# Kernel optimization log

Hardware: AMD Instinct MI355X
Metric: run time of the kernel (lower is better)

Reference implementation:

```python
import jax, jax.numpy as jnp
import numpy as np

D_K = 64

def setup_inputs() -> dict:
    key = jax.random.key(0)
    ks = jax.random.split(key, 8)
    B, C, H, W = 4, 256, 40, 40
    d_k, d_g, n_rel = 64, 64, 16
    s = lambda fan_in: 1.0 / np.sqrt(fan_in)
    return {
        "x":  jax.random.normal(ks[0], (B, C, H, W), jnp.float32),
        "Wq": jax.random.normal(ks[1], (C, d_k), jnp.float32) * s(C),
        "bq": jnp.zeros((d_k,), jnp.float32),
        "Wk": jax.random.normal(ks[2], (C, d_k), jnp.float32) * s(C),
        "bk": jnp.zeros((d_k,), jnp.float32),
        "Wv": jax.random.normal(ks[3], (C, C), jnp.float32) * s(C),
        "bv": jnp.zeros((C,), jnp.float32),
        "Wg1": jax.random.normal(ks[4], (4, d_g), jnp.float32) * s(4),
        "bg1": jnp.zeros((d_g,), jnp.float32),
        "Wg2": jax.random.normal(ks[5], (d_g, d_g), jnp.float32) * s(d_g),
        "bg2": jnp.zeros((d_g,), jnp.float32),
        "Wgr": jax.random.normal(ks[6], (d_g, n_rel), jnp.float32) * s(d_g),
        "bgr": jnp.zeros((n_rel,), jnp.float32),
    }

def reference(x, Wq, bq, Wk, bk, Wv, bv, Wg1, bg1, Wg2, bg2, Wgr, bgr):
    B, C, H, W = x.shape
    N = H * W
    # [B, N, C] feature tokens
    feats = jnp.transpose(x, (0, 2, 3, 1)).reshape(B, N, C)
    # pseudo-bboxes: (x, y, 1, 1) per pixel
    yy, xx = jnp.meshgrid(jnp.arange(H), jnp.arange(W), indexing="ij")
    bboxes = jnp.stack(
        [xx.astype(jnp.float32), yy.astype(jnp.float32),
         jnp.ones((H, W), jnp.float32), jnp.ones((H, W), jnp.float32)],
        axis=-1).reshape(N, 4)
    # pairwise geometric features [N, N, 4]: diff[m, n] = bboxes[n] - bboxes[m]
    diff = bboxes[None, :, :] - bboxes[:, None, :]
    geo = jnp.log(jnp.abs(diff) + 1e-8)
    # geo embedding MLP -> relation weights
    e = jax.nn.relu(geo @ Wg1 + bg1)            # [N, N, d_g]
    e = jax.nn.relu(e @ Wg2 + bg2)              # [N, N, d_g]
    w_g = jax.nn.relu(e @ Wgr + bgr)            # [N, N, n_rel]
    w_g_mean = w_g.mean(axis=2)                 # [N, N]
    # appearance attention
    q = feats @ Wq + bq                         # [B, N, d_k]
    k = feats @ Wk + bk                         # [B, N, d_k]
    w_a = jax.nn.softmax(jnp.einsum("bnd,bmd->bnm", q, k) / jnp.sqrt(jnp.float32(D_K)), axis=2)
    w_mn = w_a * w_g_mean[None]                 # [B, N, N]
    v = feats @ Wv + bv                         # [B, N, C]
    rel = jnp.einsum("bnm,bmc->bnc", w_mn, v)
    aug = feats + rel
    return jnp.transpose(aug.reshape(B, H, W, C), (0, 3, 1, 2))
```

## Files before the change

kernel.cpp:

```cpp
#include <hip/hip_runtime.h>
#include <hip/hip_bf16.h>
#include <math.h>

#define NTOK 1600
#define CDIM 256
#define DK   64

typedef __attribute__((ext_vector_type(8))) short bf16x8;
typedef __attribute__((ext_vector_type(4))) float f32x4;

__device__ inline unsigned short f2bf(float v) {
    unsigned int u = __float_as_uint(v);
    unsigned int r = (u + 0x7fffu + ((u >> 16) & 1u)) >> 16;
    return (unsigned short)r;
}

__global__ __launch_bounds__(256) void geo_table_kernel(
    const float* __restrict__ W1, const float* __restrict__ b1,
    const float* __restrict__ W2, const float* __restrict__ b2,
    const float* __restrict__ Wgr, const float* __restrict__ bgr,
    float* __restrict__ table)
{
    __shared__ float e1s[4][64];
    __shared__ float e2s[4][64];
    int t = threadIdx.x;
    int w = t >> 6, j = t & 63;
    int idx = blockIdx.x * 4 + w;
    int ady = idx / 40, adx = idx % 40;
    float g0 = logf((float)adx + 1e-8f);
    float g1 = logf((float)ady + 1e-8f);
    float gc = logf(1e-8f);

    float e1 = fmaxf(g0*W1[j] + g1*W1[64+j] + gc*(W1[128+j]+W1[192+j]) + b1[j], 0.f);
    e1s[w][j] = e1;
    __syncthreads();

    float e2 = b2[j];
    #pragma unroll 8
    for (int i = 0; i < 64; ++i) e2 += e1s[w][i] * W2[i*64 + j];
    e2 = fmaxf(e2, 0.f);
    e2s[w][j] = e2;
    __syncthreads();

    int r = j & 15, q = j >> 4;
    float v = (q == 0) ? bgr[r] : 0.f;
    #pragma unroll
    for (int i = 0; i < 16; ++i) v += e2s[w][q*16 + i] * Wgr[(q*16 + i)*16 + r];
    v += __shfl_xor(v, 16); v += __shfl_xor(v, 32);
    v = fmaxf(v, 0.f);
    v += __shfl_xor(v, 1); v += __shfl_xor(v, 2);
    v += __shfl_xor(v, 4); v += __shfl_xor(v, 8);
    if (j == 0) table[idx] = v * (1.f / 16.f);
}

__global__ __launch_bounds__(256) void qkv_kernel(
    const float* __restrict__ x,
    const float* __restrict__ Wq, const float* __restrict__ bq,
    const float* __restrict__ Wk, const float* __restrict__ bk,
    const float* __restrict__ Wv, const float* __restrict__ bv,
    unsigned short* __restrict__ Qb, unsigned short* __restrict__ Kb,
    unsigned short* __restrict__ Vt)
{
    const int N = NTOK;
    int bx = blockIdx.x, jt = blockIdx.y, b = blockIdx.z;
    const float* Wm; const float* bias; int jb, stride;
    if (jt == 0)      { Wm = Wq; bias = bq; jb = 0;         stride = 64;  }
    else if (jt == 1) { Wm = Wk; bias = bk; jb = 0;         stride = 64;  }
    else              { Wm = Wv; bias = bv; jb = (jt-2)*64; stride = 256; }

    __shared__ __align__(16) unsigned short As[64*72];
    __shared__ __align__(16) unsigned short Bs[64*72];

    int t = threadIdx.x;
    int w = t >> 6, l = t & 63;
    int l15 = l & 15, l4 = l >> 4;
    int n0 = bx * 64;

    f32x4 acc[4];
    #pragma unroll
    for (int i = 0; i < 4; ++i) acc[i] = (f32x4){0.f,0.f,0.f,0.f};

    for (int kc = 0; kc < 4; ++kc) {
        int k0 = kc * 64;
        __syncthreads();
        #pragma unroll
        for (int p = 0; p < 4; ++p) {
            int k = p*16 + (t >> 4);
            int n4 = (t & 15) * 4;
            float4 xv = *(const float4*)&x[((size_t)(b*CDIM) + k0 + k)*N + n0 + n4];
            As[(n4+0)*72 + k] = f2bf(xv.x); As[(n4+1)*72 + k] = f2bf(xv.y);
            As[(n4+2)*72 + k] = f2bf(xv.z); As[(n4+3)*72 + k] = f2bf(xv.w);
            float4 wv = *(const float4*)&Wm[(size_t)(k0 + k)*stride + jb + n4];
            Bs[(n4+0)*72 + k] = f2bf(wv.x); Bs[(n4+1)*72 + k] = f2bf(wv.y);
            Bs[(n4+2)*72 + k] = f2bf(wv.z); Bs[(n4+3)*72 + k] = f2bf(wv.w);
        }
        __syncthreads();
        #pragma unroll
        for (int ks = 0; ks < 2; ++ks) {
            bf16x8 a = *(const bf16x8*)&As[(w*16 + l15)*72 + ks*32 + l4*8];
            #pragma unroll
            for (int jt4 = 0; jt4 < 4; ++jt4) {
                bf16x8 bf = *(const bf16x8*)&Bs[(jt4*16 + l15)*72 + ks*32 + l4*8];
                acc[jt4] = __builtin_amdgcn_mfma_f32_16x16x32_bf16(a, bf, acc[jt4], 0, 0, 0);
            }
        }
    }

    if (jt <= 1) {
        unsigned short* outb = (jt == 0 ? Qb : Kb) + (size_t)b*N*DK;
        float scale = (jt == 0) ? 0.125f : 1.0f;
        #pragma unroll
        for (int jt4 = 0; jt4 < 4; ++jt4) {
            int j = jt4*16 + l15;
            float bb = bias[j];
            #pragma unroll
            for (int r = 0; r < 4; ++r) {
                int n = n0 + w*16 + l4*4 + r;
                outb[(size_t)n*DK + j] = f2bf((acc[jt4][r] + bb) * scale);
            }
        }
    } else {
        __syncthreads();
        unsigned short* sv = (w < 2 ? As : Bs) + (w & 1) * (64*20);
        #pragma unroll
        for (int jt4 = 0; jt4 < 4; ++jt4) {
            int j = jt4*16 + l15;
            float bb = bias[jb + j];
            #pragma unroll
            for (int r = 0; r < 4; ++r)
                sv[j*20 + l4*4 + r] = f2bf(acc[jt4][r] + bb);
        }
        __syncthreads();
        int c = l;
        uint2 lo0 = *(const uint2*)&sv[c*20 + 0];
        uint2 lo1 = *(const uint2*)&sv[c*20 + 4];
        uint2 hi0 = *(const uint2*)&sv[c*20 + 8];
        uint2 hi1 = *(const uint2*)&sv[c*20 + 12];
        unsigned short* vrow = Vt + ((size_t)b*CDIM + jb + c)*N + n0 + w*16;
        *(uint4*)(vrow)     = make_uint4(lo0.x, lo0.y, lo1.x, lo1.y);
        *(uint4*)(vrow + 8) = make_uint4(hi0.x, hi0.y, hi1.x, hi1.y);
    }
}

__global__ __launch_bounds__(256) void attn_kernel(
    const float* __restrict__ x, const float* __restrict__ gtab,
    const unsigned short* __restrict__ Qb, const unsigned short* __restrict__ Kb,
    const unsigned short* __restrict__ Vt, float* __restrict__ out)
{
    const int N = NTOK, C = CDIM;
    int b = blockIdx.y, n0 = blockIdx.x * 16;
    int t = threadIdx.x;
    int w = t >> 6, l = t & 63;
    int l15 = l & 15, l4 = l >> 4;

    __shared__ __align__(16) unsigned short Pl[4][16*72];
    __shared__ float sh_g[NTOK];
    __shared__ float outs[16][260];
    __shared__ float zs[16];

    for (int p = t; p < NTOK; p += 256) sh_g[p] = gtab[p];
    for (int p = t; p < 16*260; p += 256) ((float*)outs)[p] = 0.f;
    if (t < 16) zs[t] = 0.f;

    const unsigned short* qrow = &Qb[((size_t)b*N + n0 + l15)*DK + l4*8];
    bf16x8 qa0 = *(const bf16x8*)qrow;
    bf16x8 qa1 = *(const bf16x8*)(qrow + 32);

    f32x4 acc[16];
    #pragma unroll
    for (int i = 0; i < 16; ++i) acc[i] = (f32x4){0.f,0.f,0.f,0.f};
    float z[4] = {0.f, 0.f, 0.f, 0.f};

    int yn[4], xn[4];
    #pragma unroll
    for (int r = 0; r < 4; ++r) {
        int n = n0 + l4*4 + r;
        yn[r] = n / 40; xn[r] = n - 40*yn[r];
    }

    __syncthreads();

    unsigned short* Pw = &Pl[w][0];

    for (int cc = w; cc < 25; cc += 4) {
        int m0 = cc * 64;
        #pragma unroll
        for (int tt = 0; tt < 4; ++tt) {
            int mg = m0 + tt*16 + l15;
            const unsigned short* kbase = &Kb[((size_t)b*N + mg)*DK + l4*8];
            bf16x8 kb0 = *(const bf16x8*)kbase;
            bf16x8 kb1 = *(const bf16x8*)(kbase + 32);
            f32x4 s4 = (f32x4){0.f,0.f,0.f,0.f};
            s4 = __builtin_amdgcn_mfma_f32_16x16x32_bf16(qa0, kb0, s4, 0, 0, 0);
            s4 = __builtin_amdgcn_mfma_f32_16x16x32_bf16(qa1, kb1, s4, 0, 0, 0);
            int ym = mg / 40, xm = mg - 40*ym;
            #pragma unroll
            for (int r = 0; r < 4; ++r) {
                float e = __expf(s4[r]);
                z[r] += e;
                int ady = ym - yn[r]; ady = ady < 0 ? -ady : ady;
                int adx = xm - xn[r]; adx = adx < 0 ? -adx : adx;
                Pw[(l4*4 + r)*72 + tt*16 + l15] = f2bf(e * sh_g[ady*40 + adx]);
            }
        }
        bf16x8 pa0 = *(const bf16x8*)&Pw[l15*72 + l4*8];
        bf16x8 pa1 = *(const bf16x8*)&Pw[l15*72 + 32 + l4*8];
        #pragma unroll
        for (int ct = 0; ct < 16; ++ct) {
            const unsigned short* vb = &Vt[((size_t)b*C + ct*16 + l15)*N + m0 + l4*8];
            bf16x8 v0 = *(const bf16x8*)vb;
            bf16x8 v1 = *(const bf16x8*)(vb + 32);
            acc[ct] = __builtin_amdgcn_mfma_f32_16x16x32_bf16(pa0, v0, acc[ct], 0, 0, 0);
            acc[ct] = __builtin_amdgcn_mfma_f32_16x16x32_bf16(pa1, v1, acc[ct], 0, 0, 0);
        }
    }

    #pragma unroll
    for (int r = 0; r < 4; ++r) {
        float v = z[r];
        v += __shfl_xor(v, 1); v += __shfl_xor(v, 2);
        v += __shfl_xor(v, 4); v += __shfl_xor(v, 8);
        if (l15 == 0) atomicAdd(&zs[l4*4 + r], v);
    }
    #pragma unroll
    for (int ct = 0; ct < 16; ++ct)
        #pragma unroll
        for (int r = 0; r < 4; ++r)
            atomicAdd(&outs[l4*4 + r][ct*16 + l15], acc[ct][r]);
    __syncthreads();

    int r2 = t & 15;
    float invz = 1.f / zs[r2];
    #pragma unroll
    for (int p = 0; p < 16; ++p) {
        int c2 = p*16 + (t >> 4);
        size_t gi = ((size_t)b*C + c2)*N + n0 + r2;
        out[gi] = x[gi] + outs[r2][c2] * invz;
    }
}

extern "C" void kernel_launch(void* const* d_in, const int* in_sizes, int n_in,
                              void* d_out, int out_size, void* d_ws, size_t ws_size,
                              hipStream_t stream)
{
    const float* x   = (const float*)d_in[0];
    const float* Wq  = (const float*)d_in[1];
    const float* bq  = (const float*)d_in[2];
    const float* Wk  = (const float*)d_in[3];
    const float* bk  = (const float*)d_in[4];
    const float* Wv  = (const float*)d_in[5];
    const float* bv  = (const float*)d_in[6];
    const float* Wg1 = (const float*)d_in[7];
    const float* bg1 = (const float*)d_in[8];
    const float* Wg2 = (const float*)d_in[9];
    const float* bg2 = (const float*)d_in[10];
    const float* Wgr = (const float*)d_in[11];
    const float* bgr = (const float*)d_in[12];

    char* ws = (char*)d_ws;
    float* table       = (float*)ws;
    unsigned short* Qb = (unsigned short*)(ws + 8192);
    unsigned short* Kb = (unsigned short*)(ws + 8192 + 819200);
    unsigned short* Vt = (unsigned short*)(ws + 8192 + 2*819200);

    geo_table_kernel<<<dim3(400), dim3(256), 0, stream>>>(Wg1, bg1, Wg2, bg2, Wgr, bgr, table);
    qkv_kernel<<<dim3(25, 6, 4), dim3(256), 0, stream>>>(x, Wq, bq, Wk, bk, Wv, bv, Qb, Kb, Vt);
    attn_kernel<<<dim3(100, 4), dim3(256), 0, stream>>>(x, table, Qb, Kb, Vt, (float*)d_out);
}
```

Before: 204.5 us.

## Use 8 waves per attention block over 32-key chunks and coalesce Vt stores

The attention kernel goes from 4 to 8 wavefronts per block, with each wave handling 32-key chunks (one MFMA per channel tile) instead of 64-key chunks. This doubles the in-block parallelism over keys and trims the per-iteration P buffer. In the QKV kernel, the transposed V tile is staged through one shared buffer with stride 68 and written back as fully coalesced 16-byte rows. The cost is more LDS atomics when the 8 waves reduce their partial outputs and more register pressure under the 512-thread launch bound.

```diff
diff --git a/kernel.cpp b/kernel.cpp
--- a/kernel.cpp
+++ b/kernel.cpp
@@ -121,28 +121,27 @@
         }
     } else {
         __syncthreads();
-        unsigned short* sv = (w < 2 ? As : Bs) + (w & 1) * (64*20);
+        unsigned short* sv = As;
         #pragma unroll
         for (int jt4 = 0; jt4 < 4; ++jt4) {
             int j = jt4*16 + l15;
             float bb = bias[jb + j];
             #pragma unroll
             for (int r = 0; r < 4; ++r)
-                sv[j*20 + l4*4 + r] = f2bf(acc[jt4][r] + bb);
-        }
-        __syncthreads();
-        int c = l;
-        uint2 lo0 = *(const uint2*)&sv[c*20 + 0];
-        uint2 lo1 = *(const uint2*)&sv[c*20 + 4];
-        uint2 hi0 = *(const uint2*)&sv[c*20 + 8];
-        uint2 hi1 = *(const uint2*)&sv[c*20 + 12];
-        unsigned short* vrow = Vt + ((size_t)b*CDIM + jb + c)*N + n0 + w*16;
-        *(uint4*)(vrow)     = make_uint4(lo0.x, lo0.y, lo1.x, lo1.y);
-        *(uint4*)(vrow + 8) = make_uint4(hi0.x, hi0.y, hi1.x, hi1.y);
-    }
-}
-
-__global__ __launch_bounds__(256) void attn_kernel(
+                sv[j*68 + w*16 + l4*4 + r] = f2bf(acc[jt4][r] + bb);
+        }
+        __syncthreads();
+        #pragma unroll
+        for (int p = 0; p < 2; ++p) {
+            int c   = p*32 + (t >> 3);
+            int off = (t & 7) * 8;
+            uint4 v = *(const uint4*)&sv[c*68 + off];
+            *(uint4*)&Vt[((size_t)b*CDIM + jb + c)*N + n0 + off] = v;
+        }
+    }
+}
+
+__global__ __launch_bounds__(512) void attn_kernel(
     const float* __restrict__ x, const float* __restrict__ gtab,
     const unsigned short* __restrict__ Qb, const unsigned short* __restrict__ Kb,
     const unsigned short* __restrict__ Vt, float* __restrict__ out)
@@ -153,13 +152,13 @@
     int w = t >> 6, l = t & 63;
     int l15 = l & 15, l4 = l >> 4;
 
-    __shared__ __align__(16) unsigned short Pl[4][16*72];
+    __shared__ __align__(16) unsigned short Pl[8][16*40];
     __shared__ float sh_g[NTOK];
     __shared__ float outs[16][260];
     __shared__ float zs[16];
 
-    for (int p = t; p < NTOK; p += 256) sh_g[p] = gtab[p];
-    for (int p = t; p < 16*260; p += 256) ((float*)outs)[p] = 0.f;
+    for (int p = t; p < NTOK;   p += 512) sh_g[p] = gtab[p];
+    for (int p = t; p < 16*260; p += 512) ((float*)outs)[p] = 0.f;
     if (t < 16) zs[t] = 0.f;
 
     const unsigned short* qrow = &Qb[((size_t)b*N + n0 + l15)*DK + l4*8];
@@ -182,10 +181,10 @@
 
     unsigned short* Pw = &Pl[w][0];
 
-    for (int cc = w; cc < 25; cc += 4) {
-        int m0 = cc * 64;
-        #pragma unroll
-        for (int tt = 0; tt < 4; ++tt) {
+    for (int u = w; u < 50; u += 8) {
+        int m0 = u * 32;
+        #pragma unroll
+        for (int tt = 0; tt < 2; ++tt) {
             int mg = m0 + tt*16 + l15;
             const unsigned short* kbase = &Kb[((size_t)b*N + mg)*DK + l4*8];
             bf16x8 kb0 = *(const bf16x8*)kbase;
@@ -200,18 +199,15 @@
                 z[r] += e;
                 int ady = ym - yn[r]; ady = ady < 0 ? -ady : ady;
                 int adx = xm - xn[r]; adx = adx < 0 ? -adx : adx;
-                Pw[(l4*4 + r)*72 + tt*16 + l15] = f2bf(e * sh_g[ady*40 + adx]);
+                Pw[(l4*4 + r)*40 + tt*16 + l15] = f2bf(e * sh_g[ady*40 + adx]);
             }
         }
-        bf16x8 pa0 = *(const bf16x8*)&Pw[l15*72 + l4*8];
-        bf16x8 pa1 = *(const bf16x8*)&Pw[l15*72 + 32 + l4*8];
+        bf16x8 pa = *(const bf16x8*)&Pw[l15*40 + l4*8];
         #pragma unroll
         for (int ct = 0; ct < 16; ++ct) {
             const unsigned short* vb = &Vt[((size_t)b*C + ct*16 + l15)*N + m0 + l4*8];
             bf16x8 v0 = *(const bf16x8*)vb;
-            bf16x8 v1 = *(const bf16x8*)(vb + 32);
-            acc[ct] = __builtin_amdgcn_mfma_f32_16x16x32_bf16(pa0, v0, acc[ct], 0, 0, 0);
-            acc[ct] = __builtin_amdgcn_mfma_f32_16x16x32_bf16(pa1, v1, acc[ct], 0, 0, 0);
+            acc[ct] = __builtin_amdgcn_mfma_f32_16x16x32_bf16(pa, v0, acc[ct], 0, 0, 0);
         }
     }
 
@@ -230,10 +226,11 @@
     __syncthreads();
 
     int r2 = t & 15;
+    int cg = t >> 4;
     float invz = 1.f / zs[r2];
     #pragma unroll
-    for (int p = 0; p < 16; ++p) {
-        int c2 = p*16 + (t >> 4);
+    for (int p = 0; p < 8; ++p) {
+        int c2 = p*32 + cg;
         size_t gi = ((size_t)b*C + c2)*N + n0 + r2;
         out[gi] = x[gi] + outs[r2][c2] * invz;
     }
@@ -265,5 +262,5 @@
 
     geo_table_kernel<<<dim3(400), dim3(256), 0, stream>>>(Wg1, bg1, Wg2, bg2, Wgr, bgr, table);
     qkv_kernel<<<dim3(25, 6, 4), dim3(256), 0, stream>>>(x, Wq, bq, Wk, bk, Wv, bv, Qb, Kb, Vt);
-    attn_kernel<<<dim3(100, 4), dim3(256), 0, stream>>>(x, table, Qb, Kb, Vt, (float*)d_out);
-}
+    attn_kernel<<<dim3(100, 4), dim3(512), 0, stream>>>(x, table, Qb, Kb, Vt, (float*)d_out);
+}
```

Result: slower. 240.5 us (+17.6%).
